# Optimization experiments

Measured on AMD Instinct MI355X. Metric: run time of the kernel, lower is better.

## Reference

```python
import jax, jax.numpy as jnp
import numpy as np

LL = 1 << 20            # Fastfood padded size (power of 2 >= DD)
DD = 1024 * 768         # out_features * in_features
OUT, IN = 1024, 768


def fwht(v):
    """Unnormalized fast Walsh-Hadamard transform over a length-2^k vector."""
    n = v.shape[0]
    h = 1
    while h < n:
        v = v.reshape(-1, 2, h)
        v = jnp.concatenate([v[:, 0] + v[:, 1], v[:, 0] - v[:, 1]], axis=-1)
        h *= 2
    return v.reshape(n)


def setup_inputs() -> dict:
    key = jax.random.key(0)
    ks = jax.random.split(key, 7)
    x = jax.random.normal(ks[0], (8, 2048, IN), dtype=jnp.float32)
    theta = jax.random.normal(ks[1], (2048,), dtype=jnp.float32)
    W_0 = jax.random.normal(ks[2], (OUT, IN), dtype=jnp.float32) * 0.02
    b = jax.random.normal(ks[3], (OUT,), dtype=jnp.float32) * 0.02
    # Rademacher +/-1 diagonal
    BB = (jax.random.bernoulli(ks[4], 0.5, (LL,)).astype(jnp.float32) * 2.0 - 1.0)
    GG = jax.random.normal(ks[5], (LL,), dtype=jnp.float32)
    Pi = jax.random.permutation(ks[6], LL).astype(jnp.int64)
    return {"x": x, "theta": theta, "W_0": W_0, "b": b, "BB": BB, "GG": GG, "Pi": Pi}


def reference(x, theta, W_0, b, BB, GG, Pi):
    # pad intrinsic parameter to LL (theta.numel() < LL branch)
    theta_pad = jnp.zeros((LL,), dtype=theta.dtype).at[: theta.shape[0]].set(theta)
    # Fastfood: H B theta -> permute -> G diag -> H
    v = fwht(BB * theta_pad)
    v = v[Pi] * GG
    v = fwht(v)
    divisor = jnp.sqrt(LL * jnp.sum(GG * GG))
    update_vec = v[:DD] / (divisor * np.sqrt(float(DD) / LL))
    W_eff = W_0 + update_vec.reshape(OUT, IN)
    return jnp.einsum("bsi,oi->bso", x, W_eff) + b
```

## Files before the change

### kernel.cpp

```cpp
#include <hip/hip_runtime.h>
#include <hip/hip_bf16.h>


#define LL (1 << 20)
#define DD (1024 * 768)
#define OUTF 1024
#define INF 768
#define MROWS 16384

typedef __attribute__((ext_vector_type(8))) short s16x8;
typedef __attribute__((ext_vector_type(4))) float f32x4;
typedef __attribute__((ext_vector_type(16))) float f32x16;

__device__ __forceinline__ unsigned short f2bf(float f) {
    union { float f; unsigned u; } v; v.f = f;
    unsigned r = v.u + 0x7FFF + ((v.u >> 16) & 1);
    return (unsigned short)(r >> 16);
}

__device__ __forceinline__ unsigned cvt_pk_bf16(float lo, float hi) {
    unsigned r;
    asm("v_cvt_pk_bf16_f32 %0, %1, %2" : "=v"(r) : "v"(lo), "v"(hi));
    return r;
}

__global__ __launch_bounds__(1024)
void k3_gather_fwht_lo(const int* __restrict__ Pi, const float* __restrict__ GG,
                       const float* __restrict__ BB, const float* __restrict__ theta,
                       const float* __restrict__ X, ushort* __restrict__ XB,
                       f32x4* __restrict__ T2, float* __restrict__ partial) {
    __shared__ float r01s[2048];
    __shared__ f32x4 sA[1024];
    __shared__ float sB[4 * 1028];
    __shared__ float ws[16];
    const int t = threadIdx.x;
    const int s_r = t >> 8, tt = t & 255, lane = t & 63;
    const int row = blockIdx.x * 4 + s_r;

    const int4   pv = ((const int4*)Pi)[row * 256 + tt];
    const float4 gv = ((const float4*)GG)[row * 256 + tt];

    float w0 = BB[t] * theta[t];
    float w1 = BB[t + 1024] * theta[t + 1024];
    #pragma unroll
    for (int j = 0; j < 6; j++) {
        const float sgn = ((lane >> j) & 1) ? -1.0f : 1.0f;
        float o0 = __shfl_xor(w0, 1 << j, 64);
        float o1 = __shfl_xor(w1, 1 << j, 64);
        w0 = fmaf(sgn, w0, o0);
        w1 = fmaf(sgn, w1, o1);
    }
    float2* sr = (float2*)sB;
    sr[t] = make_float2(w0, w1);
    __syncthreads();
    {
        const int b = t & ~192;
        const float2 q00 = sr[b], q10 = sr[b + 64], q01 = sr[b + 128], q11 = sr[b + 192];
        const float s6 = (t & 64) ? -1.0f : 1.0f;
        const float s7 = (t & 128) ? -1.0f : 1.0f;
        w0 = (q00.x + s7 * q01.x) + s6 * (q10.x + s7 * q11.x);
        w1 = (q00.y + s7 * q01.y) + s6 * (q10.y + s7 * q11.y);
    }
    __syncthreads();
    sr[t] = make_float2(w0, w1);
    float g2 = gv.x * gv.x + gv.y * gv.y + gv.z * gv.z + gv.w * gv.w;
    #pragma unroll
    for (int o = 32; o > 0; o >>= 1) g2 += __shfl_down(g2, o, 64);
    if (lane == 0) ws[t >> 6] = g2;
    __syncthreads();
    {
        const int b = t & ~768;
        const float2 q00 = sr[b], q10 = sr[b + 256], q01 = sr[b + 512], q11 = sr[b + 768];
        const float s8 = (t & 256) ? -1.0f : 1.0f;
        const float s9 = (t & 512) ? -1.0f : 1.0f;
        w0 = (q00.x + s9 * q01.x) + s8 * (q10.x + s9 * q11.x);
        w1 = (q00.y + s9 * q01.y) + s8 * (q10.y + s9 * q11.y);
    }
    r01s[t] = w0;
    r01s[1024 + t] = w1;
    __syncthreads();

    float v[4];
    {
        int p; float g;
        p = pv.x; g = gv.x;
        v[0] = (r01s[p & 1023] + (((p >> 10) & 1) ? -1.0f : 1.0f) * r01s[1024 + (p & 1023)]) * g;
        p = pv.y; g = gv.y;
        v[1] = (r01s[p & 1023] + (((p >> 10) & 1) ? -1.0f : 1.0f) * r01s[1024 + (p & 1023)]) * g;
        p = pv.z; g = gv.z;
        v[2] = (r01s[p & 1023] + (((p >> 10) & 1) ? -1.0f : 1.0f) * r01s[1024 + (p & 1023)]) * g;
        p = pv.w; g = gv.w;
        v[3] = (r01s[p & 1023] + (((p >> 10) & 1) ? -1.0f : 1.0f) * r01s[1024 + (p & 1023)]) * g;
    }
    float a;
    a = v[0]; v[0] = a + v[1]; v[1] = a - v[1];
    a = v[2]; v[2] = a + v[3]; v[3] = a - v[3];
    a = v[0]; v[0] = a + v[2]; v[2] = a - v[2];
    a = v[1]; v[1] = a + v[3]; v[3] = a - v[3];
    #pragma unroll
    for (int j = 0; j < 6; j++) {
        const float sgn = ((lane >> j) & 1) ? -1.0f : 1.0f;
        #pragma unroll
        for (int c = 0; c < 4; c++) {
            float o = __shfl_xor(v[c], 1 << j, 64);
            v[c] = fmaf(sgn, v[c], o);
        }
    }
    {
        f32x4 vv; vv.x = v[0]; vv.y = v[1]; vv.z = v[2]; vv.w = v[3];
        sA[t] = vv;
    }
    __syncthreads();
    {
        const int b = t & ~192;
        const f32x4 q00 = sA[b];
        const f32x4 q10 = sA[b + 64];
        const f32x4 q01 = sA[b + 128];
        const f32x4 q11 = sA[b + 192];
        const float s8 = (tt & 64) ? -1.0f : 1.0f;
        const float s9 = (tt & 128) ? -1.0f : 1.0f;
        #pragma unroll
        for (int c = 0; c < 4; c++)
            v[c] = (q00[c] + s9 * q01[c]) + s8 * (q10[c] + s9 * q11[c]);
    }
    if (t == 0) {
        float s = 0;
        #pragma unroll
        for (int i = 0; i < 16; i++) s += ws[i];
        partial[blockIdx.x] = s;
    }
    {
        f32x4 vv; vv.x = v[0]; vv.y = v[1]; vv.z = v[2]; vv.w = v[3];
        *(f32x4*)&sB[s_r * 1028 + 4 * tt] = vv;
    }
    __syncthreads();
    {
        const int rl = t & 3;
        const int lo4 = t >> 2;
        const f32x4 w = *(const f32x4*)&sB[rl * 1028 + lo4 * 4];
        T2[(size_t)lo4 * 1024 + blockIdx.x * 4 + rl] = w;
    }

    {
        const f32x4* X4 = (const f32x4*)X;
        s16x8* O = (s16x8*)XB;
        size_t u = (size_t)blockIdx.x * 3072 + t;
        #pragma unroll
        for (int j = 0; j < 3; j++, u += 1024) {
            const f32x4 A4 = X4[2 * u];
            const f32x4 B4 = X4[2 * u + 1];
            union { s16x8 v; unsigned w4[4]; } o;
            o.w4[0] = cvt_pk_bf16(A4.x, A4.y);
            o.w4[1] = cvt_pk_bf16(A4.z, A4.w);
            o.w4[2] = cvt_pk_bf16(B4.x, B4.y);
            o.w4[3] = cvt_pk_bf16(B4.z, B4.w);
            O[u] = o.v;
        }
    }
}

__global__ __launch_bounds__(1024)
void k4_fwht_hi(const f32x4* __restrict__ T2, const float* __restrict__ partial,
                const float* __restrict__ W0, ushort* __restrict__ WB,
                const float* __restrict__ X, ushort* __restrict__ XB) {
    __shared__ f32x4 sx[1024];
    __shared__ float rw[17];
    const int t = threadIdx.x;
    const int g = blockIdx.x;
    const int lane = t & 63;

    float pr = 0.0f;
    if (t < 256) pr = partial[t];
    #pragma unroll
    for (int o = 32; o > 0; o >>= 1) pr += __shfl_down(pr, o, 64);
    if (t < 256 && lane == 0) rw[t >> 6] = pr;

    f32x4 vv = T2[(size_t)g * 1024 + t];
    #pragma unroll
    for (int j = 0; j < 6; j++) {
        const float sgn = ((lane >> j) & 1) ? -1.0f : 1.0f;
        #pragma unroll
        for (int c = 0; c < 4; c++) {
            float o = __shfl_xor(vv[c], 1 << j, 64);
            vv[c] = fmaf(sgn, vv[c], o);
        }
    }
    sx[t] = vv;
    __syncthreads();
    if (t == 0) rw[16] = rw[0] + rw[1] + rw[2] + rw[3];
    {
        const int b = t & ~192;
        const f32x4 q00 = sx[b];
        const f32x4 q10 = sx[b + 64];
        const f32x4 q01 = sx[b + 128];
        const f32x4 q11 = sx[b + 192];
        const float s6 = (t & 64) ? -1.0f : 1.0f;
        const float s7 = (t & 128) ? -1.0f : 1.0f;
        #pragma unroll
        for (int c = 0; c < 4; c++)
            vv[c] = (q00[c] + s7 * q01[c]) + s6 * (q10[c] + s7 * q11[c]);
    }
    __syncthreads();
    sx[t] = vv;
    __syncthreads();
    {
        const int b = t & ~768;
        const f32x4 q00 = sx[b];
        const f32x4 q10 = sx[b + 256];
        const f32x4 q01 = sx[b + 512];
        const f32x4 q11 = sx[b + 768];
        const float s8 = (t & 256) ? -1.0f : 1.0f;
        const float s9 = (t & 512) ? -1.0f : 1.0f;
        #pragma unroll
        for (int c = 0; c < 4; c++)
            vv[c] = (q00[c] + s9 * q01[c]) + s8 * (q10[c] + s9 * q11[c]);
    }
    if (t < 768) {
        const float scale = rsqrtf(rw[16] * (float)DD);
        const size_t d = (size_t)t * 1024 + 4 * g;
        const float4 w = *(const float4*)&W0[d];
        ushort4 o;
        o.x = f2bf(w.x + vv.x * scale);
        o.y = f2bf(w.y + vv.y * scale);
        o.z = f2bf(w.z + vv.z * scale);
        o.w = f2bf(w.w + vv.w * scale);
        *(ushort4*)&WB[d] = o;
    }

    {
        const f32x4* X4 = (const f32x4*)X;
        s16x8* O = (s16x8*)XB;
        size_t u = 786432 + (size_t)g * 3072 + t;
        #pragma unroll
        for (int j = 0; j < 3; j++, u += 1024) {
            const f32x4 A4 = X4[2 * u];
            const f32x4 B4 = X4[2 * u + 1];
            union { s16x8 v; unsigned w4[4]; } o;
            o.w4[0] = cvt_pk_bf16(A4.x, A4.y);
            o.w4[1] = cvt_pk_bf16(A4.z, A4.w);
            o.w4[2] = cvt_pk_bf16(B4.x, B4.y);
            o.w4[3] = cvt_pk_bf16(B4.z, B4.w);
            O[u] = o.v;
        }
    }
}

#define BM 128
#define BN 128
#define BK 64
#define KITERS (INF / BK)

__global__ __launch_bounds__(256)
void k7_gemm(const ushort* __restrict__ A, const ushort* __restrict__ B,
             const float* __restrict__ bias, float* __restrict__ C) {
    __shared__ ushort As[2][BM * BK];
    __shared__ ushort Bs[2][BN * BK];
    const int tid  = threadIdx.x;
    const int lane = tid & 63;
    const int wave = tid >> 6;
    const int m0 = blockIdx.x * BM;
    const int n0 = blockIdx.y * BN;
    const int wm = (wave & 1) * 64;
    const int wn = (wave >> 1) * 64;

    const int fr_row = lane & 31;
    const int fr_kh  = lane >> 5;

    f32x16 acc[2][2];
    #pragma unroll
    for (int i = 0; i < 2; i++)
        #pragma unroll
        for (int j = 0; j < 2; j++) acc[i][j] = (f32x16)(0.0f);

    auto stage = [&](int bsel, int kt) {
        #pragma unroll
        for (int i = 0; i < 4; i++) {
            const int s   = i * 256 + tid;
            const int row = s >> 3;
            const int kc  = (s & 7) ^ (row & 7);
            const ushort* ga = A + (size_t)(m0 + row) * INF + kt + kc * 8;
            const ushort* gb = B + (size_t)(n0 + row) * INF + kt + kc * 8;
            __builtin_amdgcn_global_load_lds(
                (const __attribute__((address_space(1))) void*)ga,
                (__attribute__((address_space(3))) void*)&As[bsel][i * 2048 + wave * 512], 16, 0, 0);
            __builtin_amdgcn_global_load_lds(
                (const __attribute__((address_space(1))) void*)gb,
                (__attribute__((address_space(3))) void*)&Bs[bsel][i * 2048 + wave * 512], 16, 0, 0);
        }
    };

    stage(0, 0);
    __syncthreads();

    for (int t = 0; t < KITERS; t++) {
        const int cur = t & 1;
        if (t + 1 < KITERS) stage(cur ^ 1, (t + 1) * BK);

        const ushort* Ab = As[cur];
        const ushort* Bb = Bs[cur];
        #pragma unroll
        for (int ks = 0; ks < 4; ks++) {
            const int kc = ks * 2 + fr_kh;
            s16x8 af[2], bf[2];
            #pragma unroll
            for (int mi = 0; mi < 2; mi++) {
                const int r = wm + mi * 32 + fr_row;
                af[mi] = *(const s16x8*)&Ab[(r * 8 + (kc ^ (r & 7))) * 8];
            }
            #pragma unroll
            for (int ni = 0; ni < 2; ni++) {
                const int r = wn + ni * 32 + fr_row;
                bf[ni] = *(const s16x8*)&Bb[(r * 8 + (kc ^ (r & 7))) * 8];
            }
            #pragma unroll
            for (int mi = 0; mi < 2; mi++)
                #pragma unroll
                for (int ni = 0; ni < 2; ni++)
                    acc[mi][ni] = __builtin_amdgcn_mfma_f32_32x32x16_bf16(
                        af[mi], bf[ni], acc[mi][ni], 0, 0, 0);
        }
        __syncthreads();
    }

    const int ccol = lane & 31;
    const int rbase = (lane >> 5) * 4;
    #pragma unroll
    for (int ni = 0; ni < 2; ni++) {
        const int n = n0 + wn + ni * 32 + ccol;
        const float bv = bias[n];
        #pragma unroll
        for (int mi = 0; mi < 2; mi++) {
            const int mb = m0 + wm + mi * 32 + rbase;
            #pragma unroll
            for (int r = 0; r < 16; r++) {
                const int m = mb + (r & 3) + 8 * (r >> 2);
                C[(size_t)m * OUTF + n] = acc[mi][ni][r] + bv;
            }
        }
    }
}

extern "C" void kernel_launch(void* const* d_in, const int* in_sizes, int n_in,
                              void* d_out, int out_size, void* d_ws, size_t ws_size,
                              hipStream_t stream) {
    (void)in_sizes; (void)n_in; (void)out_size; (void)ws_size;
    const float* x     = (const float*)d_in[0];
    const float* theta = (const float*)d_in[1];
    const float* W0    = (const float*)d_in[2];
    const float* bias  = (const float*)d_in[3];
    const float* BB    = (const float*)d_in[4];
    const float* GG    = (const float*)d_in[5];
    const int*   Pi    = (const int*)d_in[6];
    float* out = (float*)d_out;

    char* ws = (char*)d_ws;
    ushort* XB   = (ushort*)ws;
    f32x4*  T2   = (f32x4*)(ws + 25165824);
    ushort* WB   = (ushort*)(ws + 29360128);
    float*  PART = (float*)(ws + 30932992);

    k3_gather_fwht_lo<<<256, 1024, 0, stream>>>(Pi, GG, BB, theta, x, XB, T2, PART);
    k4_fwht_hi      <<<256, 1024, 0, stream>>>(T2, PART, W0, WB, x, XB);
    k7_gemm<<<dim3(MROWS/BM, OUTF/BN), 256, 0, stream>>>(XB, WB, bias, out);
}
```

Before: 162.1 us.

## Enlarge GEMM tile to 256x256 with 8 waves and interleaved prefetch

Grows the bf16 GEMM block tile from 128x128 to 256x256 with 512 threads (8 waves in a 2x4 grid, each computing 128x64). B fragments are loaded once per k-tile, and the next tile's A and B loads are spread across the first sub-steps. MFMA clusters are wrapped in s_setprio and separated by barriers. The aim is better operand reuse and less global traffic per FLOP. The cost is 128 KB of LDS, more accumulator registers, and only 256 blocks, which may hurt occupancy and load balance.

```diff
diff --git a/kernel.cpp b/kernel.cpp
--- a/kernel.cpp
+++ b/kernel.cpp
@@ -245,12 +245,12 @@
     }
 }
 
-#define BM 128
-#define BN 128
+#define BM 256
+#define BN 256
 #define BK 64
-#define KITERS (INF / BK)
-
-__global__ __launch_bounds__(256)
+#define KTILES (INF / BK)
+
+__global__ __launch_bounds__(512)
 void k7_gemm(const ushort* __restrict__ A, const ushort* __restrict__ B,
              const float* __restrict__ bias, float* __restrict__ C) {
     __shared__ ushort As[2][BM * BK];
@@ -258,66 +258,90 @@
     const int tid  = threadIdx.x;
     const int lane = tid & 63;
     const int wave = tid >> 6;
+    const int wr   = wave >> 2;
+    const int wc   = wave & 3;
     const int m0 = blockIdx.x * BM;
     const int n0 = blockIdx.y * BN;
-    const int wm = (wave & 1) * 64;
-    const int wn = (wave >> 1) * 64;
 
     const int fr_row = lane & 31;
     const int fr_kh  = lane >> 5;
 
-    f32x16 acc[2][2];
-    #pragma unroll
-    for (int i = 0; i < 2; i++)
+    f32x16 acc[4][2];
+    #pragma unroll
+    for (int i = 0; i < 4; i++)
         #pragma unroll
         for (int j = 0; j < 2; j++) acc[i][j] = (f32x16)(0.0f);
 
-    auto stage = [&](int bsel, int kt) {
-        #pragma unroll
-        for (int i = 0; i < 4; i++) {
-            const int s   = i * 256 + tid;
+    auto stage_half = [&](ushort* Ls, const ushort* G, int grow0, int kt, int h) {
+        #pragma unroll
+        for (int j = 0; j < 2; j++) {
+            const int s   = h * 1024 + j * 512 + tid;
             const int row = s >> 3;
             const int kc  = (s & 7) ^ (row & 7);
-            const ushort* ga = A + (size_t)(m0 + row) * INF + kt + kc * 8;
-            const ushort* gb = B + (size_t)(n0 + row) * INF + kt + kc * 8;
+            const ushort* g = G + (size_t)(grow0 + row) * INF + kt * BK + kc * 8;
             __builtin_amdgcn_global_load_lds(
-                (const __attribute__((address_space(1))) void*)ga,
-                (__attribute__((address_space(3))) void*)&As[bsel][i * 2048 + wave * 512], 16, 0, 0);
-            __builtin_amdgcn_global_load_lds(
-                (const __attribute__((address_space(1))) void*)gb,
-                (__attribute__((address_space(3))) void*)&Bs[bsel][i * 2048 + wave * 512], 16, 0, 0);
+                (const __attribute__((address_space(1))) void*)g,
+                (__attribute__((address_space(3))) void*)
+                    &Ls[(h * 1024 + j * 512 + wave * 64) * 8], 16, 0, 0);
         }
     };
 
-    stage(0, 0);
-    __syncthreads();
-
-    for (int t = 0; t < KITERS; t++) {
+    stage_half(As[0], A, m0, 0, 0);
+    stage_half(As[0], A, m0, 0, 1);
+    stage_half(Bs[0], B, n0, 0, 0);
+    stage_half(Bs[0], B, n0, 0, 1);
+    __syncthreads();
+
+    for (int t = 0; t < KTILES; t++) {
         const int cur = t & 1;
-        if (t + 1 < KITERS) stage(cur ^ 1, (t + 1) * BK);
-
         const ushort* Ab = As[cur];
         const ushort* Bb = Bs[cur];
-        #pragma unroll
-        for (int ks = 0; ks < 4; ks++) {
-            const int kc = ks * 2 + fr_kh;
-            s16x8 af[2], bf[2];
+        ushort* An = As[cur ^ 1];
+        ushort* Bn = Bs[cur ^ 1];
+        const bool pf = (t + 1 < KTILES);
+
+        s16x8 bfr[2][4];
+        #pragma unroll
+        for (int p = 0; p < 4; p++) {
+            if (p == 0) {
+                #pragma unroll
+                for (int ni = 0; ni < 2; ni++) {
+                    const int r = wc * 64 + ni * 32 + fr_row;
+                    #pragma unroll
+                    for (int ks = 0; ks < 4; ks++) {
+                        const int kc = ks * 2 + fr_kh;
+                        bfr[ni][ks] = *(const s16x8*)&Bb[(r * 8 + (kc ^ (r & 7))) * 8];
+                    }
+                }
+            }
+            s16x8 af[4];
+            {
+                const int r = wr * 128 + p * 32 + fr_row;
+                #pragma unroll
+                for (int ks = 0; ks < 4; ks++) {
+                    const int kc = ks * 2 + fr_kh;
+                    af[ks] = *(const s16x8*)&Ab[(r * 8 + (kc ^ (r & 7))) * 8];
+                }
+            }
+            if (pf) {
+                if (p == 0) {
+                    stage_half(An, A, m0, t + 1, 0);
+                    stage_half(An, A, m0, t + 1, 1);
+                } else if (p == 1) {
+                    stage_half(Bn, B, n0, t + 1, 0);
+                    stage_half(Bn, B, n0, t + 1, 1);
+                }
+            }
+            __builtin_amdgcn_s_setprio(1);
             #pragma unroll
-            for (int mi = 0; mi < 2; mi++) {
-                const int r = wm + mi * 32 + fr_row;
-                af[mi] = *(const s16x8*)&Ab[(r * 8 + (kc ^ (r & 7))) * 8];
-            }
-            #pragma unroll
-            for (int ni = 0; ni < 2; ni++) {
-                const int r = wn + ni * 32 + fr_row;
-                bf[ni] = *(const s16x8*)&Bb[(r * 8 + (kc ^ (r & 7))) * 8];
-            }
-            #pragma unroll
-            for (int mi = 0; mi < 2; mi++)
-                #pragma unroll
-                for (int ni = 0; ni < 2; ni++)
-                    acc[mi][ni] = __builtin_amdgcn_mfma_f32_32x32x16_bf16(
-                        af[mi], bf[ni], acc[mi][ni], 0, 0, 0);
+            for (int ks = 0; ks < 4; ks++) {
+                acc[p][0] = __builtin_amdgcn_mfma_f32_32x32x16_bf16(
+                    af[ks], bfr[0][ks], acc[p][0], 0, 0, 0);
+                acc[p][1] = __builtin_amdgcn_mfma_f32_32x32x16_bf16(
+                    af[ks], bfr[1][ks], acc[p][1], 0, 0, 0);
+            }
+            __builtin_amdgcn_s_setprio(0);
+            if (p < 3) __builtin_amdgcn_s_barrier();
         }
         __syncthreads();
     }
@@ -326,11 +350,11 @@
     const int rbase = (lane >> 5) * 4;
     #pragma unroll
     for (int ni = 0; ni < 2; ni++) {
-        const int n = n0 + wn + ni * 32 + ccol;
+        const int n = n0 + wc * 64 + ni * 32 + ccol;
         const float bv = bias[n];
         #pragma unroll
-        for (int mi = 0; mi < 2; mi++) {
-            const int mb = m0 + wm + mi * 32 + rbase;
+        for (int mi = 0; mi < 4; mi++) {
+            const int mb = m0 + wr * 128 + mi * 32 + rbase;
             #pragma unroll
             for (int r = 0; r < 16; r++) {
                 const int m = mb + (r & 3) + 8 * (r >> 2);
@@ -361,5 +385,5 @@
 
     k3_gather_fwht_lo<<<256, 1024, 0, stream>>>(Pi, GG, BB, theta, x, XB, T2, PART);
     k4_fwht_hi      <<<256, 1024, 0, stream>>>(T2, PART, W0, WB, x, XB);
-    k7_gemm<<<dim3(MROWS/BM, OUTF/BN), 256, 0, stream>>>(XB, WB, bias, out);
-}
+    k7_gemm<<<dim3(MROWS/BM, OUTF/BN), 512, 0, stream>>>(XB, WB, bias, out);
+}
```

New measurement: 159.7 us. Within noise of the previous version (-1.5%).
